# Optimization experiments

Measured on AMD Instinct MI355X. Metric: run time of the kernel, lower is better.

Reference implementation:

```python
import jax, jax.numpy as jnp
import numpy as np

B, N_IN, N_E, N_I, N_OUT, T = 131072, 128, 128, 64, 128, 8


def setup_inputs() -> dict:
    key = jax.random.key(0)
    k0, k1, k2, k3, k4 = jax.random.split(key, 5)
    x = jax.random.normal(k0, (B, N_IN), dtype=jnp.float32)
    # nn.Linear weights are [out_features, in_features]; original init is uniform(0,1).
    # Scale by 1/fan_in to keep the relu recurrence numerically bounded over T steps.
    W_in2E = jax.random.uniform(k1, (N_E, N_IN), dtype=jnp.float32) / N_IN
    W_I2E = jax.random.uniform(k2, (N_E, N_I), dtype=jnp.float32) / N_I
    W_E2I = jax.random.uniform(k3, (N_I, N_E), dtype=jnp.float32) / N_E
    W_E2Out = jax.random.uniform(k4, (N_OUT, N_E), dtype=jnp.float32) / N_E
    return {"x": x, "W_in2E": W_in2E, "W_I2E": W_I2E, "W_E2I": W_E2I,
            "W_E2Out": W_E2Out, "num_timesteps": T}


def reference(x, W_in2E, W_I2E, W_E2I, W_E2Out, num_timesteps):
    # tau = 1 for every population, so each step: state = sum_proj W @ pre_activity,
    # activity = relu(state + bias) with bias = 0 (learn_bias defaults False).
    # Population order within a step: InputE -> H1E -> H1I -> OutE, so H1E uses
    # H1I's activity from the previous step (the recurrent carry).
    ff = x @ W_in2E.T                                  # [B, N_E], constant over steps

    def step(actI, _):
        actE = jax.nn.relu(ff + actI @ W_I2E.T)        # H1.E
        actI_new = jax.nn.relu(actE @ W_E2I.T)         # H1.I (uses current actE)
        out = jax.nn.relu(actE @ W_E2Out.T)            # Output.E
        return actI_new, out

    actI0 = jnp.zeros((x.shape[0], W_I2E.shape[1]), dtype=x.dtype)
    _, outs = jax.lax.scan(step, actI0, None, length=num_timesteps)
    return outs[-1]                                    # output_pop.activity after last step
```

## Files before the change

### kernel.cpp

```cpp
#include <hip/hip_runtime.h>
#include <hip/hip_bf16.h>


typedef __bf16 bf16x8_t __attribute__((ext_vector_type(8)));
typedef float f32x4_t __attribute__((ext_vector_type(4)));
typedef unsigned int uintx4_t __attribute__((ext_vector_type(4)));

#define THREADS 512

#define OFF_WIN2E 0
#define OFF_WI2E 32768
#define OFF_WE2I 49152
#define OFF_WE2OUT 65536
#define SMEM_TOTAL 98304

__device__ __forceinline__ f32x4_t mfma16(bf16x8_t a, bf16x8_t b, f32x4_t c) {
  return __builtin_amdgcn_mfma_f32_16x16x32_bf16(a, b, c, 0, 0, 0);
}

__device__ __forceinline__ void swap32(unsigned int& x, unsigned int& y) {
  asm("v_permlane32_swap_b32 %0, %1" : "+v"(x), "+v"(y));
}
__device__ __forceinline__ void swap16(unsigned int& x, unsigned int& y) {
  asm("v_permlane16_swap_b32 %0, %1" : "+v"(x), "+v"(y));
}

__device__ __forceinline__ unsigned int pack2_relu(float a, float b) {
  unsigned short lo = __builtin_bit_cast(unsigned short, (__bf16)fmaxf(a, 0.f));
  unsigned short hi = __builtin_bit_cast(unsigned short, (__bf16)fmaxf(b, 0.f));
  return (unsigned int)lo | ((unsigned int)hi << 16);
}

__device__ __forceinline__ bf16x8_t remap2(const f32x4_t& t0,
                                           const f32x4_t& t1) {
  unsigned int A0 = pack2_relu(t0[0], t0[1]);
  unsigned int A1 = pack2_relu(t0[2], t0[3]);
  unsigned int B0 = pack2_relu(t1[0], t1[1]);
  unsigned int B1 = pack2_relu(t1[2], t1[3]);
  swap32(A0, B0);
  swap16(A0, B0);
  swap32(A1, B1);
  swap16(A1, B1);
  return __builtin_bit_cast(bf16x8_t, (uintx4_t){A0, A1, B0, B1});
}

__device__ __forceinline__ bf16x8_t cvt8(float4 v0, float4 v1) {
  bf16x8_t h;
  h[0] = (__bf16)v0.x; h[1] = (__bf16)v0.y;
  h[2] = (__bf16)v0.z; h[3] = (__bf16)v0.w;
  h[4] = (__bf16)v1.x; h[5] = (__bf16)v1.y;
  h[6] = (__bf16)v1.z; h[7] = (__bf16)v1.w;
  return h;
}

__device__ __forceinline__ bf16x8_t ldsfrag(const char* smem, int off, int fi,
                                            int lane) {
  return *reinterpret_cast<const bf16x8_t*>(smem + off + (fi * 64 + lane) * 16);
}

template <int NMT, int NKS, int COLS>
__device__ __forceinline__ void stage_frags(const float* __restrict__ W,
                                            char* dst, int tid) {
  constexpr int SLOTS = NMT * NKS * 64;
#pragma unroll
  for (int it = 0; it < SLOTS / THREADS; ++it) {
    int slot = it * THREADS + tid;
    int lane = slot & 63;
    int fi = slot >> 6;
    int mt = fi / NKS, ks = fi % NKS;
    int cc = lane & 15, hh = lane >> 4;
    const float* src = W + (mt * 16 + cc) * COLS + ks * 32 + hh * 8;
    float4 v0 = *reinterpret_cast<const float4*>(src);
    float4 v1 = *reinterpret_cast<const float4*>(src + 4);
    *reinterpret_cast<bf16x8_t*>(dst + slot * 16) = cvt8(v0, v1);
  }
}

__global__ __launch_bounds__(THREADS, 2) void unet_fused(
    const float* __restrict__ x,
    const float* __restrict__ Win2E,
    const float* __restrict__ WI2E,
    const float* __restrict__ WE2I,
    const float* __restrict__ WE2Out,
    const int* __restrict__ Tptr,
    float* __restrict__ out) {
  extern __shared__ char smem[];
  const int tid = threadIdx.x;

  stage_frags<8, 4, 128>(Win2E, smem + OFF_WIN2E, tid);
  stage_frags<8, 2, 64>(WI2E, smem + OFF_WI2E, tid);
  stage_frags<4, 4, 128>(WE2I, smem + OFF_WE2I, tid);
  stage_frags<8, 4, 128>(WE2Out, smem + OFF_WE2OUT, tid);

  const int wid = tid >> 6, lane = tid & 63;
  const int c = lane & 15, q = lane >> 4;
  const int T = *Tptr;
  const long row0 = ((long)blockIdx.x * 8 + wid) * 16;
  const f32x4_t Z = {};

  const float* xrow = x + (row0 + c) * 128 + q * 8;
  float4 xv[8];
#pragma unroll
  for (int s = 0; s < 4; ++s) {
    xv[2 * s] = *reinterpret_cast<const float4*>(xrow + s * 32);
    xv[2 * s + 1] = *reinterpret_cast<const float4*>(xrow + s * 32 + 4);
  }

  __syncthreads();

  bf16x8_t xb[4];
#pragma unroll
  for (int s = 0; s < 4; ++s) xb[s] = cvt8(xv[2 * s], xv[2 * s + 1]);

  f32x4_t ff[8];
#pragma unroll
  for (int mt = 0; mt < 8; ++mt)
    ff[mt] = mfma16(ldsfrag(smem, OFF_WIN2E, mt * 4 + 0, lane), xb[0], Z);
#pragma unroll
  for (int s = 1; s < 4; ++s)
#pragma unroll
    for (int mt = 0; mt < 8; ++mt)
      ff[mt] = mfma16(ldsfrag(smem, OFF_WIN2E, mt * 4 + s, lane), xb[s], ff[mt]);

  bf16x8_t wi2e[8][2];
#pragma unroll
  for (int mt = 0; mt < 8; ++mt)
#pragma unroll
    for (int s = 0; s < 2; ++s)
      wi2e[mt][s] = ldsfrag(smem, OFF_WI2E, mt * 2 + s, lane);
  bf16x8_t we2i[4][4];
#pragma unroll
  for (int mt = 0; mt < 4; ++mt)
#pragma unroll
    for (int s = 0; s < 4; ++s)
      we2i[mt][s] = ldsfrag(smem, OFF_WE2I, mt * 4 + s, lane);

  f32x4_t acc_e[8];
#pragma unroll
  for (int mt = 0; mt < 8; ++mt) acc_e[mt] = ff[mt];

  for (int t = 0; t < T - 1; ++t) {
    f32x4_t acc_i[4];
#pragma unroll
    for (int s = 0; s < 4; ++s) {
      bf16x8_t ebs = remap2(acc_e[2 * s], acc_e[2 * s + 1]);
#pragma unroll
      for (int mt = 0; mt < 4; ++mt)
        acc_i[mt] = mfma16(we2i[mt][s], ebs, s == 0 ? Z : acc_i[mt]);
    }
#pragma unroll
    for (int s = 0; s < 2; ++s) {
      bf16x8_t ibs = remap2(acc_i[2 * s], acc_i[2 * s + 1]);
#pragma unroll
      for (int mt = 0; mt < 8; ++mt)
        acc_e[mt] = mfma16(wi2e[mt][s], ibs, s == 0 ? ff[mt] : acc_e[mt]);
    }
  }

  bf16x8_t eb[4];
#pragma unroll
  for (int s = 0; s < 4; ++s) eb[s] = remap2(acc_e[2 * s], acc_e[2 * s + 1]);
#pragma unroll
  for (int mt = 0; mt < 8; ++mt) {
    f32x4_t o = mfma16(ldsfrag(smem, OFF_WE2OUT, mt * 4 + 0, lane), eb[0], Z);
#pragma unroll
    for (int s = 1; s < 4; ++s)
      o = mfma16(ldsfrag(smem, OFF_WE2OUT, mt * 4 + s, lane), eb[s], o);
    f32x4_t r;
#pragma unroll
    for (int j = 0; j < 4; ++j) r[j] = fmaxf(o[j], 0.f);
    *reinterpret_cast<f32x4_t*>(out + (row0 + c) * 128 + mt * 16 + q * 4) = r;
  }
}

extern "C" void kernel_launch(void* const* d_in, const int* in_sizes, int n_in,
                              void* d_out, int out_size, void* d_ws,
                              size_t ws_size, hipStream_t stream) {
  const float* x = (const float*)d_in[0];
  const float* Win2E = (const float*)d_in[1];
  const float* WI2E = (const float*)d_in[2];
  const float* WE2I = (const float*)d_in[3];
  const float* WE2Out = (const float*)d_in[4];
  const int* Tptr = (const int*)d_in[5];
  float* out = (float*)d_out;
  (void)n_in; (void)out_size; (void)d_ws; (void)ws_size;

  const int B = in_sizes[0] / 128;
  (void)hipFuncSetAttribute(reinterpret_cast<const void*>(unet_fused),
                            hipFuncAttributeMaxDynamicSharedMemorySize,
                            SMEM_TOTAL);
  dim3 grid(B / 128), block(THREADS);
  unet_fused<<<grid, block, SMEM_TOTAL, stream>>>(x, Win2E, WI2E, WE2I, WE2Out,
                                                  Tptr, out);
}
```

Before: 77.13 us.

## Process two 16-row tiles per wave and read recurrent weights from LDS

Each wave now handles 32 batch rows as two independent 16-row tiles, so every weight fragment loaded is reused for two MFMAs and the two recurrence chains interleave to hide MFMA latency. The recurrent weights are no longer kept in registers and are reloaded from LDS on each step, which frees VGPRs for the doubled accumulators. The grid is halved to match. This trades extra LDS traffic and fewer blocks (512 on the device) for more instruction-level parallelism in the serial recurrence.

```diff
diff --git a/kernel.cpp b/kernel.cpp
--- a/kernel.cpp
+++ b/kernel.cpp
@@ -95,81 +95,95 @@
   const int wid = tid >> 6, lane = tid & 63;
   const int c = lane & 15, q = lane >> 4;
   const int T = *Tptr;
-  const long row0 = ((long)blockIdx.x * 8 + wid) * 16;
+  const long base = ((long)blockIdx.x * 8 + wid) * 32;
   const f32x4_t Z = {};
 
-  const float* xrow = x + (row0 + c) * 128 + q * 8;
-  float4 xv[8];
-#pragma unroll
-  for (int s = 0; s < 4; ++s) {
-    xv[2 * s] = *reinterpret_cast<const float4*>(xrow + s * 32);
-    xv[2 * s + 1] = *reinterpret_cast<const float4*>(xrow + s * 32 + 4);
+  float4 xv[2][8];
+#pragma unroll
+  for (int u = 0; u < 2; ++u) {
+    const float* xrow = x + (base + u * 16 + c) * 128 + q * 8;
+#pragma unroll
+    for (int s = 0; s < 4; ++s) {
+      xv[u][2 * s] = *reinterpret_cast<const float4*>(xrow + s * 32);
+      xv[u][2 * s + 1] = *reinterpret_cast<const float4*>(xrow + s * 32 + 4);
+    }
   }
 
   __syncthreads();
 
-  bf16x8_t xb[4];
-#pragma unroll
-  for (int s = 0; s < 4; ++s) xb[s] = cvt8(xv[2 * s], xv[2 * s + 1]);
-
-  f32x4_t ff[8];
-#pragma unroll
-  for (int mt = 0; mt < 8; ++mt)
-    ff[mt] = mfma16(ldsfrag(smem, OFF_WIN2E, mt * 4 + 0, lane), xb[0], Z);
-#pragma unroll
-  for (int s = 1; s < 4; ++s)
-#pragma unroll
-    for (int mt = 0; mt < 8; ++mt)
-      ff[mt] = mfma16(ldsfrag(smem, OFF_WIN2E, mt * 4 + s, lane), xb[s], ff[mt]);
-
-  bf16x8_t wi2e[8][2];
-#pragma unroll
-  for (int mt = 0; mt < 8; ++mt)
-#pragma unroll
-    for (int s = 0; s < 2; ++s)
-      wi2e[mt][s] = ldsfrag(smem, OFF_WI2E, mt * 2 + s, lane);
-  bf16x8_t we2i[4][4];
-#pragma unroll
-  for (int mt = 0; mt < 4; ++mt)
+  bf16x8_t xb[2][4];
+#pragma unroll
+  for (int u = 0; u < 2; ++u)
 #pragma unroll
     for (int s = 0; s < 4; ++s)
-      we2i[mt][s] = ldsfrag(smem, OFF_WE2I, mt * 4 + s, lane);
-
-  f32x4_t acc_e[8];
-#pragma unroll
-  for (int mt = 0; mt < 8; ++mt) acc_e[mt] = ff[mt];
+      xb[u][s] = cvt8(xv[u][2 * s], xv[u][2 * s + 1]);
+
+  f32x4_t ff[2][8];
+#pragma unroll
+  for (int s = 0; s < 4; ++s)
+#pragma unroll
+    for (int mt = 0; mt < 8; ++mt) {
+      bf16x8_t a = ldsfrag(smem, OFF_WIN2E, mt * 4 + s, lane);
+#pragma unroll
+      for (int u = 0; u < 2; ++u)
+        ff[u][mt] = mfma16(a, xb[u][s], s == 0 ? Z : ff[u][mt]);
+    }
+
+  f32x4_t acc_e[2][8];
+#pragma unroll
+  for (int u = 0; u < 2; ++u)
+#pragma unroll
+    for (int mt = 0; mt < 8; ++mt) acc_e[u][mt] = ff[u][mt];
 
   for (int t = 0; t < T - 1; ++t) {
-    f32x4_t acc_i[4];
+    f32x4_t acc_i[2][4];
 #pragma unroll
     for (int s = 0; s < 4; ++s) {
-      bf16x8_t ebs = remap2(acc_e[2 * s], acc_e[2 * s + 1]);
-#pragma unroll
-      for (int mt = 0; mt < 4; ++mt)
-        acc_i[mt] = mfma16(we2i[mt][s], ebs, s == 0 ? Z : acc_i[mt]);
+      bf16x8_t e0 = remap2(acc_e[0][2 * s], acc_e[0][2 * s + 1]);
+      bf16x8_t e1 = remap2(acc_e[1][2 * s], acc_e[1][2 * s + 1]);
+#pragma unroll
+      for (int mt = 0; mt < 4; ++mt) {
+        bf16x8_t a = ldsfrag(smem, OFF_WE2I, mt * 4 + s, lane);
+        acc_i[0][mt] = mfma16(a, e0, s == 0 ? Z : acc_i[0][mt]);
+        acc_i[1][mt] = mfma16(a, e1, s == 0 ? Z : acc_i[1][mt]);
+      }
     }
 #pragma unroll
     for (int s = 0; s < 2; ++s) {
-      bf16x8_t ibs = remap2(acc_i[2 * s], acc_i[2 * s + 1]);
-#pragma unroll
-      for (int mt = 0; mt < 8; ++mt)
-        acc_e[mt] = mfma16(wi2e[mt][s], ibs, s == 0 ? ff[mt] : acc_e[mt]);
-    }
-  }
-
-  bf16x8_t eb[4];
-#pragma unroll
-  for (int s = 0; s < 4; ++s) eb[s] = remap2(acc_e[2 * s], acc_e[2 * s + 1]);
+      bf16x8_t i0 = remap2(acc_i[0][2 * s], acc_i[0][2 * s + 1]);
+      bf16x8_t i1 = remap2(acc_i[1][2 * s], acc_i[1][2 * s + 1]);
+#pragma unroll
+      for (int mt = 0; mt < 8; ++mt) {
+        bf16x8_t a = ldsfrag(smem, OFF_WI2E, mt * 2 + s, lane);
+        acc_e[0][mt] = mfma16(a, i0, s == 0 ? ff[0][mt] : acc_e[0][mt]);
+        acc_e[1][mt] = mfma16(a, i1, s == 0 ? ff[1][mt] : acc_e[1][mt]);
+      }
+    }
+  }
+
+  bf16x8_t eb[2][4];
+#pragma unroll
+  for (int u = 0; u < 2; ++u)
+#pragma unroll
+    for (int s = 0; s < 4; ++s)
+      eb[u][s] = remap2(acc_e[u][2 * s], acc_e[u][2 * s + 1]);
 #pragma unroll
   for (int mt = 0; mt < 8; ++mt) {
-    f32x4_t o = mfma16(ldsfrag(smem, OFF_WE2OUT, mt * 4 + 0, lane), eb[0], Z);
-#pragma unroll
-    for (int s = 1; s < 4; ++s)
-      o = mfma16(ldsfrag(smem, OFF_WE2OUT, mt * 4 + s, lane), eb[s], o);
-    f32x4_t r;
-#pragma unroll
-    for (int j = 0; j < 4; ++j) r[j] = fmaxf(o[j], 0.f);
-    *reinterpret_cast<f32x4_t*>(out + (row0 + c) * 128 + mt * 16 + q * 4) = r;
+    f32x4_t o[2] = {Z, Z};
+#pragma unroll
+    for (int s = 0; s < 4; ++s) {
+      bf16x8_t a = ldsfrag(smem, OFF_WE2OUT, mt * 4 + s, lane);
+#pragma unroll
+      for (int u = 0; u < 2; ++u) o[u] = mfma16(a, eb[u][s], o[u]);
+    }
+#pragma unroll
+    for (int u = 0; u < 2; ++u) {
+      f32x4_t r;
+#pragma unroll
+      for (int j = 0; j < 4; ++j) r[j] = fmaxf(o[u][j], 0.f);
+      *reinterpret_cast<f32x4_t*>(out + (base + u * 16 + c) * 128 + mt * 16 +
+                                  q * 4) = r;
+    }
   }
 }
 
@@ -189,7 +203,7 @@
   (void)hipFuncSetAttribute(reinterpret_cast<const void*>(unet_fused),
                             hipFuncAttributeMaxDynamicSharedMemorySize,
                             SMEM_TOTAL);
-  dim3 grid(B / 128), block(THREADS);
+  dim3 grid(B / 256), block(THREADS);
   unet_fused<<<grid, block, SMEM_TOTAL, stream>>>(x, Win2E, WI2E, WE2I, WE2Out,
                                                   Tptr, out);
 }
```

New measurement: 68.44 us. 1.13x faster.
